# Performance work log

Hardware: AMD Instinct MI355X
Metric: run time of the kernel (lower is better)

Reference implementation:

```python
import jax, jax.numpy as jnp
import numpy as np

B, IN_C, L, D, K, DEPTH, OUT = 16, 3, 2048, 256, 8, 4, 1
F = L // 2 + 1
EPS = 1e-5


def _hilbert_basis_rfft(grid_size, k):
    # Hilbert matrix Z[i,j] = 1/(i+j+1), symmetric PSD; take top-k eigvecs.
    i = np.arange(grid_size, dtype=np.float64)
    Z = 1.0 / (i[:, None] + i[None, :] + 1.0)
    w, V = np.linalg.eigh(Z)
    idx = np.argsort(w)[::-1][:k]
    Vt = V.T[idx]                                   # (k, L)
    Phi_f = np.fft.rfft(Vt, n=grid_size, axis=-1)   # (k, L//2+1) complex
    return Phi_f.astype(np.complex64)


def setup_inputs() -> dict:
    key = jax.random.key(0)
    ks = jax.random.split(key, 10)
    phi = _hilbert_basis_rfft(L, K)
    s = 0.05
    return {
        "x": jax.random.normal(ks[0], (B, IN_C, L), jnp.float32),
        "lift_w": jax.random.normal(ks[1], (D, IN_C + 1), jnp.float32) * s,
        "lift_b": jax.random.normal(ks[2], (D,), jnp.float32) * s,
        "theta": jax.random.normal(ks[3], (DEPTH, K, D, D), jnp.float32) * (1.0 / np.sqrt(D)),
        "ln_gamma": jnp.ones((DEPTH, D), jnp.float32),
        "ln_beta": jnp.zeros((DEPTH, D), jnp.float32),
        "glu_val_w": jax.random.normal(ks[4], (DEPTH, D, D), jnp.float32) * (1.0 / np.sqrt(D)),
        "glu_val_b": jax.random.normal(ks[5], (DEPTH, D), jnp.float32) * s,
        "glu_gate_w": jax.random.normal(ks[6], (DEPTH, D, D), jnp.float32) * (1.0 / np.sqrt(D)),
        "glu_gate_b": jax.random.normal(ks[7], (DEPTH, D), jnp.float32) * s,
        "head_w": jax.random.normal(ks[8], (OUT, D), jnp.float32) * (1.0 / np.sqrt(D)),
        "head_b": jax.random.normal(ks[9], (OUT,), jnp.float32) * s,
        "phi_real": jnp.asarray(phi.real, jnp.float32),
        "phi_imag": jnp.asarray(phi.imag, jnp.float32),
    }


def _layernorm_channels(h, gamma, beta):
    # h: (b, d, t); normalize over channel dim d (matches LayerNorm on transposed input)
    mu = jnp.mean(h, axis=1, keepdims=True)
    var = jnp.mean(jnp.square(h - mu), axis=1, keepdims=True)
    z = (h - mu) * jax.lax.rsqrt(var + EPS)
    return z * gamma[None, :, None] + beta[None, :, None]


def reference(x, lift_w, lift_b, theta, ln_gamma, ln_beta,
              glu_val_w, glu_val_b, glu_gate_w, glu_gate_b,
              head_w, head_b, phi_real, phi_imag):
    phi = phi_real + 1j * phi_imag                      # (K, F) complex
    phi_c = jnp.conj(phi)
    # add grid coordinate channel
    coords = jnp.linspace(0.0, 1.0, L, dtype=x.dtype)
    coords = jnp.broadcast_to(coords[None, None, :], (x.shape[0], 1, L))
    h = jnp.concatenate([x, coords], axis=1)            # (b, in+1, L)
    # pointwise lift (Conv1d kernel_size=1, norm=Identity)
    h = jnp.einsum("oi,bit->bot", lift_w, h) + lift_b[None, :, None]
    for i in range(DEPTH):
        z = _layernorm_channels(h, ln_gamma[i], ln_beta[i])
        Xf = jnp.fft.rfft(z, axis=-1)                   # (b, d, F) complex64
        # Exploit FFT linearity: S = sum_{l,d} Theta[l,h,d] * irfft(Xf[b,d] * conj(Phi[l]))
        #                          = irfft( sum_{l,d} Theta[l,h,d]*conj(Phi[l,f]) * Xf[b,d,f] )
        W = jnp.einsum("lhd,lf->hdf", theta[i].astype(Xf.dtype), phi_c)  # (h, d, F)
        Sf = jnp.einsum("bdf,hdf->bhf", Xf, W)          # (b, h, F)
        S = jnp.fft.irfft(Sf, n=L, axis=-1)             # (b, h, L)
        V = jnp.einsum("od,bdt->bot", glu_val_w[i], S) + glu_val_b[i][None, :, None]
        G = jax.nn.sigmoid(jnp.einsum("od,bdt->bot", glu_gate_w[i], S) + glu_gate_b[i][None, :, None])
        h = h + V * G                                   # residual + GLU
    y = jnp.einsum("od,bdt->bot", head_w, h) + head_b[None, :, None]
    return y
```

## Files before the change

kernel.cpp:

```cpp
#include <hip/hip_runtime.h>
#include <math.h>

#define NB 16
#define CIN 3
#define LL 2048
#define DD 256
#define KK 8
#define NDEPTH 4
#define FF 1025
#define FFP 1032
#define FFS 1032
#define LOGL 11

typedef _Float16 half8 __attribute__((ext_vector_type(8)));
typedef _Float16 half2v __attribute__((ext_vector_type(2)));
typedef float f32x4 __attribute__((ext_vector_type(4)));

union H8 { half8 h8; unsigned int u[4]; uint4 q; };
union H2 { _Float16 h[2]; unsigned int u; half2v v; };
union PK4 { float2 f2[4]; uint4 q[2]; };

#if defined(__has_builtin)
#if __has_builtin(__builtin_amdgcn_fdot2)
#define HAS_FDOT2 1
#endif
#endif

__device__ inline float fdot2_acc(unsigned int a, unsigned int b, float c){
    H2 ua, ub; ua.u = a; ub.u = b;
#ifdef HAS_FDOT2
    return __builtin_amdgcn_fdot2(ua.v, ub.v, c, false);
#else
    return c + (float)ua.h[0]*(float)ub.h[0] + (float)ua.h[1]*(float)ub.h[1];
#endif
}

__device__ inline float2 cmul(const float2 a, const float2 b){
    return make_float2(a.x*b.x - a.y*b.y, a.x*b.y + a.y*b.x);
}
__device__ inline float2 cadd(const float2 a, const float2 b){ return make_float2(a.x+b.x, a.y+b.y); }
__device__ inline float2 csub(const float2 a, const float2 b){ return make_float2(a.x-b.x, a.y-b.y); }

template<bool CONJ>
__device__ inline void r8_stage(float2* a, const float2* __restrict__ tw, int g, int s){
    const int hs = 1 << s;
    int pos = g & (hs-1);
    int grp = g >> s;
    int q = (grp << (s+3)) + pos;
    float2 ws = tw[pos << (LOGL-1-s)];
    float2 w1 = tw[pos << (LOGL-2-s)];
    float2 w2 = tw[(pos+hs) << (LOGL-2-s)];
    float2 v0 = tw[pos << (LOGL-3-s)];
    float2 v1 = tw[(pos+hs) << (LOGL-3-s)];
    float2 v2 = tw[(pos+2*hs) << (LOGL-3-s)];
    float2 v3 = tw[(pos+3*hs) << (LOGL-3-s)];
    if (CONJ){ ws.y=-ws.y; w1.y=-w1.y; w2.y=-w2.y; v0.y=-v0.y; v1.y=-v1.y; v2.y=-v2.y; v3.y=-v3.y; }
    float2 A0=a[q],      A1=a[q+hs],   A2=a[q+2*hs], A3=a[q+3*hs],
           A4=a[q+4*hs], A5=a[q+5*hs], A6=a[q+6*hs], A7=a[q+7*hs];
    float2 t;
    t=cmul(ws,A1); float2 b0=cadd(A0,t), b1=csub(A0,t);
    t=cmul(ws,A3); float2 b2=cadd(A2,t), b3=csub(A2,t);
    t=cmul(ws,A5); float2 b4=cadd(A4,t), b5=csub(A4,t);
    t=cmul(ws,A7); float2 b6=cadd(A6,t), b7=csub(A6,t);
    t=cmul(w1,b2); float2 c0=cadd(b0,t), c2=csub(b0,t);
    t=cmul(w2,b3); float2 c1=cadd(b1,t), c3=csub(b1,t);
    t=cmul(w1,b6); float2 c4=cadd(b4,t), c6=csub(b4,t);
    t=cmul(w2,b7); float2 c5=cadd(b5,t), c7=csub(b5,t);
    t=cmul(v0,c4); a[q]      =cadd(c0,t); a[q+4*hs]=csub(c0,t);
    t=cmul(v1,c5); a[q+hs]   =cadd(c1,t); a[q+5*hs]=csub(c1,t);
    t=cmul(v2,c6); a[q+2*hs] =cadd(c2,t); a[q+6*hs]=csub(c2,t);
    t=cmul(v3,c7); a[q+3*hs] =cadd(c3,t); a[q+7*hs]=csub(c3,t);
}

template<bool CONJ>
__device__ inline void r4_final(float2* a, const float2* __restrict__ tw, int g){
    int pos = g;
    float2 ws = tw[pos << 1];
    float2 w1 = tw[pos];
    float2 w2 = tw[pos + 512];
    if (CONJ){ ws.y=-ws.y; w1.y=-w1.y; w2.y=-w2.y; }
    float2 a0 = a[pos], a1 = a[pos+512], a2 = a[pos+1024], a3 = a[pos+1536];
    float2 t1 = cmul(ws, a1), t3 = cmul(ws, a3);
    float2 x0 = cadd(a0,t1), x1 = csub(a0,t1);
    float2 x2 = cadd(a2,t3), x3 = csub(a2,t3);
    float2 u1 = cmul(w1, x2), u2 = cmul(w2, x3);
    a[pos]      = cadd(x0,u1);
    a[pos+1024] = csub(x0,u1);
    a[pos+512]  = cadd(x1,u2);
    a[pos+1536] = csub(x1,u2);
}

__global__ void twiddle_kernel(float2* __restrict__ tw){
    int j = blockIdx.x*blockDim.x + threadIdx.x;
    if (j < LL/2){
        double ang = -2.0*3.14159265358979323846*(double)j/(double)LL;
        tw[j] = make_float2((float)cos(ang), (float)sin(ang));
    }
}

__global__ void conv_w_kernel(const float* __restrict__ wv, const float* __restrict__ wg,
                              _Float16* __restrict__ Wf){
    int idx = blockIdx.x*256 + threadIdx.x;
    int layer = idx >> 17;
    int vg = (idx >> 16) & 1;
    int rem = idx & 65535;
    int o = rem >> 8, d = rem & 255;
    const float* src = (vg ? wg : wv) + ((size_t)layer << 16);
    float val = src[(o << 8) + d];
    size_t dst = ((((size_t)(layer*2+vg)*16 + (o>>4))*8 + (d>>5))*64
                  + (o&15) + 16*((d>>3)&3))*8 + (d&7);
    Wf[dst] = (_Float16)val;
}

__global__ void transpose_theta16_kernel(const float* __restrict__ in,
                                         unsigned int* __restrict__ out){
    __shared__ float tile[2][32][33];
    int m = blockIdx.z;
    int layer = m >> 2, lp = m & 3;
    int d0 = blockIdx.x*32, h0 = blockIdx.y*32;
    int tx = threadIdx.x & 31, ty = threadIdx.x >> 5;
    const float* src0 = in + ((size_t)layer*KK + 2*lp)*DD*DD;
    const float* src1 = src0 + (size_t)DD*DD;
    #pragma unroll
    for (int i = 0; i < 4; ++i){
        tile[0][ty + i*8][tx] = src0[(size_t)(h0 + ty + i*8)*DD + d0 + tx];
        tile[1][ty + i*8][tx] = src1[(size_t)(h0 + ty + i*8)*DD + d0 + tx];
    }
    __syncthreads();
    #pragma unroll
    for (int i = 0; i < 4; ++i){
        H2 p;
        p.h[0] = (_Float16)tile[0][tx][ty + i*8];
        p.h[1] = (_Float16)tile[1][tx][ty + i*8];
        out[((size_t)m*DD + d0 + ty + i*8)*DD + h0 + tx] = p.u;
    }
}

__global__ __launch_bounds__(256) void lift_ln_kernel(const float* __restrict__ x,
        const float* __restrict__ lw, const float* __restrict__ lb,
        const float* __restrict__ gamma, const float* __restrict__ beta,
        float* __restrict__ h, float* __restrict__ z){
    __shared__ float red[2][4][64];
    __shared__ float stat[2][64];
    __shared__ float gb[512];
    int tid = threadIdx.x;
    int t = tid & 63, dg = tid >> 6;
    int b = blockIdx.y;
    int tg = blockIdx.x*64 + t;
    gb[tid] = gamma[tid];
    gb[256 + tid] = beta[tid];
    const float* xb = x + (size_t)b*CIN*LL;
    float x0 = xb[tg], x1 = xb[LL + tg], x2 = xb[2*LL + tg];
    float coord = (float)tg * (1.0f/(LL-1));
    float hv[64];
    float s = 0.f, ss = 0.f;
    float* hp = h + (size_t)b*DD*LL + tg;
    #pragma unroll
    for (int j = 0; j < 64; ++j){
        int d = dg*64 + j;
        float4 w = *(const float4*)&lw[d*4];
        float v = lb[d];
        v = fmaf(w.x, x0, v); v = fmaf(w.y, x1, v);
        v = fmaf(w.z, x2, v); v = fmaf(w.w, coord, v);
        hv[j] = v;
        s += v; ss = fmaf(v, v, ss);
        hp[(size_t)d*LL] = v;
    }
    red[0][dg][t] = s; red[1][dg][t] = ss;
    __syncthreads();
    if (tid < 64){
        float S1 = red[0][0][tid] + red[0][1][tid] + red[0][2][tid] + red[0][3][tid];
        float S2 = red[1][0][tid] + red[1][1][tid] + red[1][2][tid] + red[1][3][tid];
        float mu = S1*(1.0f/DD);
        float var = S2*(1.0f/DD) - mu*mu;
        stat[0][tid] = mu;
        stat[1][tid] = rsqrtf(var + 1e-5f);
    }
    __syncthreads();
    float mu = stat[0][t], rs = stat[1][t];
    float* zp = z + (size_t)b*DD*LL + tg;
    #pragma unroll
    for (int j = 0; j < 64; ++j){
        int d = dg*64 + j;
        zp[(size_t)d*LL] = (hv[j] - mu)*rs*gb[d] + gb[256 + d];
    }
}

__global__ __launch_bounds__(256) void fft_fwd_pair_kernel(const float* __restrict__ in,
                                                           unsigned int* __restrict__ XfH,
                                                           const float2* __restrict__ tw){
    __shared__ float2 a[LL];
    int blk = blockIdx.x;
    const float* src0 = in + (size_t)(blk*2)*LL;
    const float* src1 = src0 + LL;
    int tid = threadIdx.x;
    #pragma unroll
    for (int i = 0; i < LL/256; ++i){
        int idx = tid + i*256;
        int rev = __brev((unsigned)idx) >> (32-LOGL);
        a[rev] = make_float2(src0[idx], src1[idx]);
    }
    __syncthreads();
    r8_stage<false>(a, tw, tid, 0);  __syncthreads();
    r8_stage<false>(a, tw, tid, 3);  __syncthreads();
    r8_stage<false>(a, tw, tid, 6);  __syncthreads();
    r4_final<false>(a, tw, tid);
    r4_final<false>(a, tw, tid + 256);
    __syncthreads();
    unsigned int* dst0 = XfH + (size_t)(blk*2)*FFP;
    unsigned int* dst1 = dst0 + FFP;
    #pragma unroll
    for (int i = 0; i < 5; ++i){
        int f = tid + i*256;
        if (f <= 1024){
            int m = (LL - f) & (LL-1);
            float2 A = a[f], B = a[m];
            H2 p0, p1;
            p0.h[0] = (_Float16)(0.5f*(A.x + B.x));
            p0.h[1] = (_Float16)(0.5f*(A.y - B.y));
            p1.h[0] = (_Float16)(0.5f*(A.y + B.y));
            p1.h[1] = (_Float16)(0.5f*(B.x - A.x));
            dst0[f] = p0.u;
            dst1[f] = p1.u;
        }
    }
    if (tid < 7){
        dst0[1025 + tid] = 0u;
        dst1[1025 + tid] = 0u;
    }
}

__global__ __launch_bounds__(256) void fft_inv_pair_kernel(const float2* __restrict__ Sf0,
                                                           unsigned int* __restrict__ Sfrag,
                                                           const float2* __restrict__ tw){
    __shared__ float2 a[LL];
    int blk = blockIdx.x;
    const float2* src0 = Sf0 + (size_t)(blk*2)*FFS;
    const float2* src1 = src0 + FFS;
    int tid = threadIdx.x;
    #pragma unroll
    for (int i = 0; i < LL/256; ++i){
        int idx = tid + i*256;
        float2 Y;
        if (idx <= 1024){
            float2 s0 = src0[idx], s1 = src1[idx];
            Y = make_float2(s0.x - s1.y, s0.y + s1.x);
        } else {
            int m = LL - idx;
            float2 s0 = src0[m], s1 = src1[m];
            Y = make_float2(s0.x + s1.y, s1.x - s0.y);
        }
        int rev = __brev((unsigned)idx) >> (32-LOGL);
        a[rev] = Y;
    }
    __syncthreads();
    r8_stage<true>(a, tw, tid, 0);  __syncthreads();
    r8_stage<true>(a, tw, tid, 3);  __syncthreads();
    r8_stage<true>(a, tw, tid, 6);  __syncthreads();
    r4_final<true>(a, tw, tid);
    r4_final<true>(a, tw, tid + 256);
    __syncthreads();
    int b = blk >> 7, dl = (blk & 127)*2;
    int kc = dl >> 5, lq4 = (dl >> 3) & 3, jh = (dl & 7) >> 1;
    unsigned int* dst = Sfrag + ((size_t)(b*8 + kc)*128)*64*4;
    const float sc = 1.0f/(float)LL;
    #pragma unroll
    for (int i = 0; i < LL/256; ++i){
        int t = tid + i*256;
        float2 v = a[t];
        H2 p;
        p.h[0] = (_Float16)(v.x*sc);
        p.h[1] = (_Float16)(v.y*sc);
        dst[(((t>>4)*64) + (t&15) + 16*lq4)*4 + jh] = p.u;
    }
}

__global__ __launch_bounds__(512, 4) void spectral7_kernel(
    const unsigned int* __restrict__ XfH,
    const unsigned int* __restrict__ th16,
    const float* __restrict__ phr, const float* __restrict__ phim,
    float2* __restrict__ Sf0){
    __shared__ unsigned int Apairs[8*64*8];
    __shared__ unsigned int phi2[2][8][4];
    int tid = threadIdx.x;
    int w = tid >> 6, lane = tid & 63;
    int hc = w & 3, fh = w >> 2;
    int n = lane & 15, kp = lane >> 4;
    int f0 = blockIdx.x * 8;
    int h0 = blockIdx.y * 64;
    int h = h0 + hc*16 + n;

    if (tid < 32){
        int ff = tid >> 2, lp = tid & 3;
        H2 a, b;
        a.h[0] = (_Float16)phr[(2*lp)*FF + f0 + ff];
        a.h[1] = (_Float16)phr[(2*lp+1)*FF + f0 + ff];
        b.h[0] = (_Float16)(-phim[(2*lp)*FF + f0 + ff]);
        b.h[1] = (_Float16)(-phim[(2*lp+1)*FF + f0 + ff]);
        phi2[0][ff][lp] = a.u;
        phi2[1][ff][lp] = b.u;
    }

    f32x4 accre[4], accim[4];
    #pragma unroll
    for (int i = 0; i < 4; ++i){
        accre[i] = (f32x4){0.f,0.f,0.f,0.f};
        accim[i] = (f32x4){0.f,0.f,0.f,0.f};
    }

    for (int kc = 0; kc < 8; ++kc){
        unsigned int th_pk[4][8];
        #pragma unroll
        for (int lp = 0; lp < 4; ++lp)
            #pragma unroll
            for (int j = 0; j < 8; ++j)
                th_pk[lp][j] = th16[((size_t)lp*DD + kc*32 + kp*8 + j)*DD + h];

        __syncthreads();
        {
            int bb = tid & 15;
            int dd = tid >> 4;
            const uint4* src = (const uint4*)(XfH + ((size_t)(bb*DD + kc*32 + dd)*FFP + f0));
            uint4 v0 = src[0], v1 = src[1];
            int L = bb + 16*(dd >> 3), j = dd & 7;
            unsigned int vv[8] = {v0.x, v0.y, v0.z, v0.w, v1.x, v1.y, v1.z, v1.w};
            #pragma unroll
            for (int ff = 0; ff < 8; ++ff){
                int A = ff*2048 + L*32 + j*4;
                A ^= ((A >> 7) & 3) << 5;
                *(unsigned int*)((char*)Apairs + A) = vv[ff];
            }
        }
        __syncthreads();

        #pragma unroll
        for (int ffl = 0; ffl < 4; ++ffl){
            int ff = fh*4 + ffl;
            unsigned int pr2[4], pi2[4];
            #pragma unroll
            for (int lp = 0; lp < 4; ++lp){
                pr2[lp] = phi2[0][ff][lp];
                pi2[lp] = phi2[1][ff][lp];
            }
            int Ab = ff*2048 + lane*32;
            Ab ^= ((Ab >> 7) & 3) << 5;
            uint4 lo = *(const uint4*)((const char*)Apairs + Ab);
            uint4 hi = *(const uint4*)((const char*)Apairs + Ab + 16);
            unsigned int dw[8] = {lo.x, lo.y, lo.z, lo.w, hi.x, hi.y, hi.z, hi.w};
            H8 Are, Aim, Anim;
            #pragma unroll
            for (int k = 0; k < 4; ++k){
                Are.u[k]  = __builtin_amdgcn_perm(dw[2*k+1], dw[2*k], 0x05040100u);
                Aim.u[k]  = __builtin_amdgcn_perm(dw[2*k+1], dw[2*k], 0x07060302u);
                Anim.u[k] = Aim.u[k] ^ 0x80008000u;
            }
            float wre[8], wim[8];
            #pragma unroll
            for (int j = 0; j < 8; ++j){
                float re = 0.f, im = 0.f;
                #pragma unroll
                for (int lp = 0; lp < 4; ++lp){
                    re = fdot2_acc(th_pk[lp][j], pr2[lp], re);
                    im = fdot2_acc(th_pk[lp][j], pi2[lp], im);
                }
                wre[j] = re; wim[j] = im;
            }
            H8 Bre, Bim;
            #pragma unroll
            for (int j = 0; j < 8; ++j){
                Bre.h8[j] = (_Float16)wre[j];
                Bim.h8[j] = (_Float16)wim[j];
            }
            accre[ffl] = __builtin_amdgcn_mfma_f32_16x16x32_f16(Are.h8,  Bre.h8, accre[ffl], 0, 0, 0);
            accre[ffl] = __builtin_amdgcn_mfma_f32_16x16x32_f16(Anim.h8, Bim.h8, accre[ffl], 0, 0, 0);
            accim[ffl] = __builtin_amdgcn_mfma_f32_16x16x32_f16(Are.h8,  Bim.h8, accim[ffl], 0, 0, 0);
            accim[ffl] = __builtin_amdgcn_mfma_f32_16x16x32_f16(Aim.h8,  Bre.h8, accim[ffl], 0, 0, 0);
        }
    }
    #pragma unroll
    for (int r = 0; r < 4; ++r){
        int bb = kp*4 + r;
        PK4 pk;
        #pragma unroll
        for (int ffl = 0; ffl < 4; ++ffl)
            pk.f2[ffl] = make_float2(accre[ffl][r], accim[ffl][r]);
        uint4* dst = (uint4*)(Sf0 + ((size_t)(bb*DD) + h)*FFS + f0 + fh*4);
        dst[0] = pk.q[0]; dst[1] = pk.q[1];
    }
}

__global__ __launch_bounds__(256) void nyq_kernel(const unsigned int* __restrict__ XfH,
    const unsigned int* __restrict__ th16,
    const float* __restrict__ phr, const float* __restrict__ phim,
    float2* __restrict__ Sf0){
    __shared__ float2 red[256];
    int tid = threadIdx.x;
    int hb = blockIdx.x, b = blockIdx.y;
    int h = hb*16 + (tid & 15);
    int dp = tid >> 4;
    float pr[KK], pi[KK];
    #pragma unroll
    for (int l = 0; l < KK; ++l){ pr[l] = phr[l*FF + 1024]; pi[l] = -phim[l*FF + 1024]; }
    float2 acc = make_float2(0.f, 0.f);
    for (int j = 0; j < 16; ++j){
        int d = dp*16 + j;
        float wre = 0.f, wim = 0.f;
        #pragma unroll
        for (int lp = 0; lp < 4; ++lp){
            H2 t; t.u = th16[((size_t)lp*DD + d)*DD + h];
            float t0 = (float)t.h[0], t1 = (float)t.h[1];
            wre = fmaf(t0, pr[2*lp], fmaf(t1, pr[2*lp+1], wre));
            wim = fmaf(t0, pi[2*lp], fmaf(t1, pi[2*lp+1], wim));
        }
        H2 u; u.u = XfH[(size_t)(b*DD + d)*FFP + 1024];
        float2 x = make_float2((float)u.h[0], (float)u.h[1]);
        acc.x = fmaf(x.x, wre, fmaf(-x.y, wim, acc.x));
        acc.y = fmaf(x.x, wim, fmaf( x.y, wre, acc.y));
    }
    red[tid] = acc;
    __syncthreads();
    if (tid < 16){
        float2 s = make_float2(0.f, 0.f);
        #pragma unroll
        for (int k = 0; k < 16; ++k){ s.x += red[tid + k*16].x; s.y += red[tid + k*16].y; }
        Sf0[((size_t)b*DD + hb*16 + tid)*FFS + 1024] = s;
    }
}

template<int MODE>
__global__ __launch_bounds__(256, 2) void glu_mfma_kernel(
    const uint4* __restrict__ Sfrag,
    const uint4* __restrict__ WfL,
    const float* __restrict__ bv, const float* __restrict__ bg,
    float* __restrict__ h, float* __restrict__ outp,
    const float* __restrict__ aux1, const float* __restrict__ aux2){
    __shared__ float sb[1024];
    __shared__ float red[2][4][4][16];
    __shared__ float stat[2][4][16];
    int tid = threadIdx.x;
    int w = tid >> 6, lane = tid & 63;
    int tl = lane & 15, lq = lane >> 4;
    int b = blockIdx.y, tb4 = blockIdx.x;

    sb[tid] = bv[tid];
    sb[256 + tid] = bg[tid];
    sb[512 + tid] = aux1[tid];
    if (MODE == 0) sb[768 + tid] = aux2[tid];
    __syncthreads();

    f32x4 aV[4][4], aG[4][4];
    #pragma unroll
    for (int mt = 0; mt < 4; ++mt)
        #pragma unroll
        for (int nt = 0; nt < 4; ++nt){
            aV[mt][nt] = (f32x4){0.f,0.f,0.f,0.f};
            aG[mt][nt] = (f32x4){0.f,0.f,0.f,0.f};
        }

    for (int kc = 0; kc < 8; ++kc){
        H8 Bf[4];
        #pragma unroll
        for (int nt = 0; nt < 4; ++nt)
            Bf[nt].q = Sfrag[((size_t)(b*8 + kc)*128 + tb4*4 + nt)*64 + lane];
        H8 Av[4], Ag[4];
        #pragma unroll
        for (int mt = 0; mt < 4; ++mt){
            int ot = w*4 + mt;
            Av[mt].q = WfL[((size_t)(ot)*8 + kc)*64 + lane];
            Ag[mt].q = WfL[((size_t)(16 + ot)*8 + kc)*64 + lane];
        }
        #pragma unroll
        for (int mt = 0; mt < 4; ++mt)
            #pragma unroll
            for (int nt = 0; nt < 4; ++nt){
                aV[mt][nt] = __builtin_amdgcn_mfma_f32_16x16x32_f16(Av[mt].h8, Bf[nt].h8, aV[mt][nt], 0, 0, 0);
                aG[mt][nt] = __builtin_amdgcn_mfma_f32_16x16x32_f16(Ag[mt].h8, Bf[nt].h8, aG[mt][nt], 0, 0, 0);
            }
    }

    #pragma unroll
    for (int mt = 0; mt < 4; ++mt){
        #pragma unroll
        for (int r = 0; r < 4; ++r){
            int o = w*64 + mt*16 + lq*4 + r;
            float bvv = sb[o], bgv = sb[256 + o];
            float* hp = h + ((size_t)(b*DD + o))*LL + tb4*64 + tl;
            #pragma unroll
            for (int nt = 0; nt < 4; ++nt){
                float v = aV[mt][nt][r] + bvv;
                float g = aG[mt][nt][r] + bgv;
                g = 1.0f/(1.0f + __expf(-g));
                float cur = hp[nt*16] + v*g;
                if (MODE == 0) hp[nt*16] = cur;
                aV[mt][nt][r] = cur;
            }
        }
    }

    float s[4], ss[4];
    #pragma unroll
    for (int nt = 0; nt < 4; ++nt){ s[nt] = 0.f; ss[nt] = 0.f; }
    #pragma unroll
    for (int mt = 0; mt < 4; ++mt)
        #pragma unroll
        for (int r = 0; r < 4; ++r){
            int o = w*64 + mt*16 + lq*4 + r;
            float wo = (MODE == 0) ? 1.0f : sb[512 + o];
            #pragma unroll
            for (int nt = 0; nt < 4; ++nt){
                float cur = aV[mt][nt][r];
                if (MODE == 0){ s[nt] += cur; ss[nt] = fmaf(cur, cur, ss[nt]); }
                else { s[nt] = fmaf(wo, cur, s[nt]); }
            }
        }
    #pragma unroll
    for (int nt = 0; nt < 4; ++nt){
        s[nt] += __shfl_xor(s[nt], 16); s[nt] += __shfl_xor(s[nt], 32);
        if (MODE == 0){ ss[nt] += __shfl_xor(ss[nt], 16); ss[nt] += __shfl_xor(ss[nt], 32); }
    }
    if (lq == 0){
        #pragma unroll
        for (int nt = 0; nt < 4; ++nt){
            red[0][w][nt][tl] = s[nt];
            if (MODE == 0) red[1][w][nt][tl] = ss[nt];
        }
    }
    __syncthreads();
    if (MODE == 0){
        if (tid < 64){
            int nt = tid >> 4, t2 = tid & 15;
            float S1 = red[0][0][nt][t2] + red[0][1][nt][t2] + red[0][2][nt][t2] + red[0][3][nt][t2];
            float S2 = red[1][0][nt][t2] + red[1][1][nt][t2] + red[1][2][nt][t2] + red[1][3][nt][t2];
            float mu = S1*(1.0f/DD);
            float var = S2*(1.0f/DD) - mu*mu;
            stat[0][nt][t2] = mu;
            stat[1][nt][t2] = rsqrtf(var + 1e-5f);
        }
        __syncthreads();
        #pragma unroll
        for (int mt = 0; mt < 4; ++mt){
            #pragma unroll
            for (int r = 0; r < 4; ++r){
                int o = w*64 + mt*16 + lq*4 + r;
                float gam = sb[512 + o], bet = sb[768 + o];
                float* zp = outp + ((size_t)(b*DD + o))*LL + tb4*64 + tl;
                #pragma unroll
                for (int nt = 0; nt < 4; ++nt){
                    float zv = (aV[mt][nt][r] - stat[0][nt][tl])*stat[1][nt][tl]*gam + bet;
                    zp[nt*16] = zv;
                }
            }
        }
    } else {
        if (tid < 64){
            int nt = tid >> 4, t2 = tid & 15;
            float S1 = red[0][0][nt][t2] + red[0][1][nt][t2] + red[0][2][nt][t2] + red[0][3][nt][t2];
            outp[(size_t)b*LL + tb4*64 + tid] = S1 + aux2[0];
        }
    }
}

extern "C" void kernel_launch(void* const* d_in, const int* in_sizes, int n_in,
                              void* d_out, int out_size, void* d_ws, size_t ws_size,
                              hipStream_t stream){
    (void)in_sizes; (void)n_in; (void)out_size; (void)ws_size;
    const float* x      = (const float*)d_in[0];
    const float* lift_w = (const float*)d_in[1];
    const float* lift_b = (const float*)d_in[2];
    const float* theta  = (const float*)d_in[3];
    const float* ln_g   = (const float*)d_in[4];
    const float* ln_b   = (const float*)d_in[5];
    const float* gvw    = (const float*)d_in[6];
    const float* gvb    = (const float*)d_in[7];
    const float* ggw    = (const float*)d_in[8];
    const float* ggb    = (const float*)d_in[9];
    const float* hw     = (const float*)d_in[10];
    const float* hb     = (const float*)d_in[11];
    const float* phr    = (const float*)d_in[12];
    const float* phim   = (const float*)d_in[13];
    float* out = (float*)d_out;

    char* ws = (char*)d_ws;
    size_t off = 0;
    float2* tw  = (float2*)(ws + off); off += (size_t)(LL/2)*sizeof(float2);
    _Float16* Wf = (_Float16*)(ws + off); off += (size_t)NDEPTH*2*DD*DD*2;
    unsigned int* th16 = (unsigned int*)(ws + off); off += (size_t)NDEPTH*4*DD*DD*4;
    off = (off + 255) & ~(size_t)255;
    float*  h   = (float*)(ws + off);  off += (size_t)NB*DD*LL*4;
    float*  z   = (float*)(ws + off);  off += (size_t)NB*DD*LL*4;
    unsigned int* XfH = (unsigned int*)(ws + off); off += (size_t)NB*DD*FFP*4;
    unsigned int* Sfrag = XfH;
    off = (off + 255) & ~(size_t)255;
    float2* Sf0 = (float2*)(ws + off); off += (size_t)NB*DD*FFS*8;

    twiddle_kernel<<<4, 256, 0, stream>>>(tw);
    conv_w_kernel<<<(NDEPTH*2*DD*DD)/256, 256, 0, stream>>>(gvw, ggw, Wf);
    transpose_theta16_kernel<<<dim3(8,8,NDEPTH*4), 256, 0, stream>>>(theta, th16);
    lift_ln_kernel<<<dim3(LL/64, NB), 256, 0, stream>>>(x, lift_w, lift_b, ln_g, ln_b, h, z);

    for (int layer = 0; layer < NDEPTH; ++layer){
        const unsigned int* thL = th16 + (size_t)layer*4*DD*DD;
        const uint4* WfL = (const uint4*)(Wf + (size_t)layer*2*DD*DD);
        fft_fwd_pair_kernel<<<NB*DD/2, 256, 0, stream>>>(z, XfH, tw);
        spectral7_kernel<<<dim3(128,4), 512, 0, stream>>>(XfH, thL, phr, phim, Sf0);
        nyq_kernel<<<dim3(16,16), 256, 0, stream>>>(XfH, thL, phr, phim, Sf0);
        fft_inv_pair_kernel<<<NB*DD/2, 256, 0, stream>>>(Sf0, Sfrag, tw);
        if (layer < NDEPTH-1){
            glu_mfma_kernel<0><<<dim3(LL/64, NB), 256, 0, stream>>>(
                (const uint4*)Sfrag, WfL,
                gvb + layer*DD, ggb + layer*DD, h, z,
                ln_g + (layer+1)*DD, ln_b + (layer+1)*DD);
        } else {
            glu_mfma_kernel<1><<<dim3(LL/64, NB), 256, 0, stream>>>(
                (const uint4*)Sfrag, WfL,
                gvb + layer*DD, ggb + layer*DD, h, out, hw, hb);
        }
    }
}
```

Before: 526.7 us.

## Store normalized activations in fp16 and refine LDS swizzle in spectral kernel

The layer-normed activation z is now written as fp16 by the lift and GLU kernels and read as packed half pairs by the forward FFT, halving that intermediate's global memory traffic. The spectral kernel's LDS swizzle gains an extra XOR bit so the two 16-byte halves of each row land in different banks, aiming to reduce bank conflicts. The cost is reduced input precision to the FFT, though the FFT output was already stored in fp16.

```diff
diff --git a/kernel.cpp b/kernel.cpp
--- a/kernel.cpp
+++ b/kernel.cpp
@@ -139,7 +139,7 @@
 __global__ __launch_bounds__(256) void lift_ln_kernel(const float* __restrict__ x,
         const float* __restrict__ lw, const float* __restrict__ lb,
         const float* __restrict__ gamma, const float* __restrict__ beta,
-        float* __restrict__ h, float* __restrict__ z){
+        float* __restrict__ h, _Float16* __restrict__ z){
     __shared__ float red[2][4][64];
     __shared__ float stat[2][64];
     __shared__ float gb[512];
@@ -178,27 +178,33 @@
     }
     __syncthreads();
     float mu = stat[0][t], rs = stat[1][t];
-    float* zp = z + (size_t)b*DD*LL + tg;
+    _Float16* zp = z + (size_t)b*DD*LL + tg;
     #pragma unroll
     for (int j = 0; j < 64; ++j){
         int d = dg*64 + j;
-        zp[(size_t)d*LL] = (hv[j] - mu)*rs*gb[d] + gb[256 + d];
-    }
-}
-
-__global__ __launch_bounds__(256) void fft_fwd_pair_kernel(const float* __restrict__ in,
+        zp[(size_t)d*LL] = (_Float16)((hv[j] - mu)*rs*gb[d] + gb[256 + d]);
+    }
+}
+
+__global__ __launch_bounds__(256) void fft_fwd_pair_kernel(const unsigned int* __restrict__ zh,
                                                            unsigned int* __restrict__ XfH,
                                                            const float2* __restrict__ tw){
     __shared__ float2 a[LL];
     int blk = blockIdx.x;
-    const float* src0 = in + (size_t)(blk*2)*LL;
-    const float* src1 = src0 + LL;
+    const unsigned int* s0 = zh + (size_t)(blk*2)*(LL/2);
+    const unsigned int* s1 = s0 + (LL/2);
     int tid = threadIdx.x;
     #pragma unroll
-    for (int i = 0; i < LL/256; ++i){
-        int idx = tid + i*256;
-        int rev = __brev((unsigned)idx) >> (32-LOGL);
-        a[rev] = make_float2(src0[idx], src1[idx]);
+    for (int i = 0; i < 4; ++i){
+        int tp = tid + i*256;
+        H2 u0, u1;
+        u0.u = s0[tp];
+        u1.u = s1[tp];
+        int t0 = 2*tp, t1 = 2*tp + 1;
+        int r0 = __brev((unsigned)t0) >> (32-LOGL);
+        int r1 = __brev((unsigned)t1) >> (32-LOGL);
+        a[r0] = make_float2((float)u0.h[0], (float)u1.h[0]);
+        a[r1] = make_float2((float)u0.h[1], (float)u1.h[1]);
     }
     __syncthreads();
     r8_stage<false>(a, tw, tid, 0);  __syncthreads();
@@ -327,8 +333,8 @@
             #pragma unroll
             for (int ff = 0; ff < 8; ++ff){
                 int A = ff*2048 + L*32 + j*4;
-                A ^= ((A >> 7) & 3) << 5;
-                *(unsigned int*)((char*)Apairs + A) = vv[ff];
+                int sw = (((A >> 7) & 3) << 5) | (((A >> 8) & 1) << 4);
+                *(unsigned int*)((char*)Apairs + (A ^ sw)) = vv[ff];
             }
         }
         __syncthreads();
@@ -343,9 +349,10 @@
                 pi2[lp] = phi2[1][ff][lp];
             }
             int Ab = ff*2048 + lane*32;
-            Ab ^= ((Ab >> 7) & 3) << 5;
+            int sw = (((Ab >> 7) & 3) << 5) | (((Ab >> 8) & 1) << 4);
+            Ab ^= sw;
             uint4 lo = *(const uint4*)((const char*)Apairs + Ab);
-            uint4 hi = *(const uint4*)((const char*)Apairs + Ab + 16);
+            uint4 hi = *(const uint4*)((const char*)Apairs + (Ab ^ 16));
             unsigned int dw[8] = {lo.x, lo.y, lo.z, lo.w, hi.x, hi.y, hi.z, hi.w};
             H8 Are, Aim, Anim;
             #pragma unroll
@@ -543,11 +550,11 @@
             for (int r = 0; r < 4; ++r){
                 int o = w*64 + mt*16 + lq*4 + r;
                 float gam = sb[512 + o], bet = sb[768 + o];
-                float* zp = outp + ((size_t)(b*DD + o))*LL + tb4*64 + tl;
+                _Float16* zp = (_Float16*)outp + ((size_t)(b*DD + o))*LL + tb4*64 + tl;
                 #pragma unroll
                 for (int nt = 0; nt < 4; ++nt){
                     float zv = (aV[mt][nt][r] - stat[0][nt][tl])*stat[1][nt][tl]*gam + bet;
-                    zp[nt*16] = zv;
+                    zp[nt*16] = (_Float16)zv;
                 }
             }
         }
@@ -587,7 +594,7 @@
     unsigned int* th16 = (unsigned int*)(ws + off); off += (size_t)NDEPTH*4*DD*DD*4;
     off = (off + 255) & ~(size_t)255;
     float*  h   = (float*)(ws + off);  off += (size_t)NB*DD*LL*4;
-    float*  z   = (float*)(ws + off);  off += (size_t)NB*DD*LL*4;
+    _Float16* zh = (_Float16*)(ws + off); off += (size_t)NB*DD*LL*2;
     unsigned int* XfH = (unsigned int*)(ws + off); off += (size_t)NB*DD*FFP*4;
     unsigned int* Sfrag = XfH;
     off = (off + 255) & ~(size_t)255;
@@ -596,19 +603,19 @@
     twiddle_kernel<<<4, 256, 0, stream>>>(tw);
     conv_w_kernel<<<(NDEPTH*2*DD*DD)/256, 256, 0, stream>>>(gvw, ggw, Wf);
     transpose_theta16_kernel<<<dim3(8,8,NDEPTH*4), 256, 0, stream>>>(theta, th16);
-    lift_ln_kernel<<<dim3(LL/64, NB), 256, 0, stream>>>(x, lift_w, lift_b, ln_g, ln_b, h, z);
+    lift_ln_kernel<<<dim3(LL/64, NB), 256, 0, stream>>>(x, lift_w, lift_b, ln_g, ln_b, h, zh);
 
     for (int layer = 0; layer < NDEPTH; ++layer){
         const unsigned int* thL = th16 + (size_t)layer*4*DD*DD;
         const uint4* WfL = (const uint4*)(Wf + (size_t)layer*2*DD*DD);
-        fft_fwd_pair_kernel<<<NB*DD/2, 256, 0, stream>>>(z, XfH, tw);
+        fft_fwd_pair_kernel<<<NB*DD/2, 256, 0, stream>>>((const unsigned int*)zh, XfH, tw);
         spectral7_kernel<<<dim3(128,4), 512, 0, stream>>>(XfH, thL, phr, phim, Sf0);
         nyq_kernel<<<dim3(16,16), 256, 0, stream>>>(XfH, thL, phr, phim, Sf0);
         fft_inv_pair_kernel<<<NB*DD/2, 256, 0, stream>>>(Sf0, Sfrag, tw);
         if (layer < NDEPTH-1){
             glu_mfma_kernel<0><<<dim3(LL/64, NB), 256, 0, stream>>>(
                 (const uint4*)Sfrag, WfL,
-                gvb + layer*DD, ggb + layer*DD, h, z,
+                gvb + layer*DD, ggb + layer*DD, h, (float*)zh,
                 ln_g + (layer+1)*DD, ln_b + (layer+1)*DD);
         } else {
             glu_mfma_kernel<1><<<dim3(LL/64, NB), 256, 0, stream>>>(
```

Measured after the change: 525.0 us (median of 2 runs). Within noise of the previous version (-0.3%).
